# Kernel tuning notes

Measured on AMD Instinct MI355X. Metric: run time of the kernel, lower is better.

The kernel has to match this reference:

```python
import jax, jax.numpy as jnp
import numpy as np
import jax.ops

N_NODES = 50000
N_EDGES = 800000
N_GRAPHS = 512
F_IN = 128
HID = 256
N_CLASSES = 1

def _xavier(key, shape):
    fan_in, fan_out = shape[0], shape[1]
    std = (2.0 / (fan_in + fan_out)) ** 0.5
    return jax.random.normal(key, shape, dtype=jnp.float32) * std

def setup_inputs() -> dict:
    key = jax.random.key(0)
    ks = jax.random.split(key, 12)
    x = jax.random.normal(ks[0], (N_NODES, F_IN), dtype=jnp.float32)
    edge_index = jax.random.randint(ks[1], (2, N_EDGES), 0, N_NODES, dtype=jnp.int64)
    batch = jnp.sort(jax.random.randint(ks[2], (N_NODES,), 0, N_GRAPHS, dtype=jnp.int64))
    return {
        'x': x, 'edge_index': edge_index, 'batch': batch,
        'W0': _xavier(ks[3], (F_IN, HID)), 'b0': jnp.zeros((HID,), jnp.float32),
        'W1': _xavier(ks[4], (HID, HID)), 'b1': jnp.zeros((HID,), jnp.float32),
        'W2': _xavier(ks[5], (HID, HID)), 'b2': jnp.zeros((HID,), jnp.float32),
        'Wm1': _xavier(ks[6], (HID, HID)), 'bm1': jnp.zeros((HID,), jnp.float32),
        'Wm2': _xavier(ks[7], (HID, N_CLASSES)), 'bm2': jnp.zeros((N_CLASSES,), jnp.float32),
    }

def _gcn_layer(h, W, b, src, dst, deg_inv_sqrt):
    # PyG GCNConv: linear -> symmetric-normalized aggregation (with self loops) -> bias
    hw = h @ W                                        # [N, out]
    norm = deg_inv_sqrt[src] * deg_inv_sqrt[dst]      # [E]
    msg = hw[src] * norm[:, None]                     # [E, out]
    agg = jax.ops.segment_sum(msg, dst, num_segments=N_NODES)
    agg = agg + hw * (deg_inv_sqrt ** 2)[:, None]     # self-loop term
    return agg + b

def reference(x, edge_index, batch, W0, b0, W1, b1, W2, b2, Wm1, bm1, Wm2, bm2):
    src, dst = edge_index[0], edge_index[1]
    # degree with added self loops (in-degree at dst)
    deg = jax.ops.segment_sum(jnp.ones((N_EDGES,), jnp.float32), dst, num_segments=N_NODES) + 1.0
    deg_inv_sqrt = jax.lax.rsqrt(deg)
    h = jax.nn.relu(_gcn_layer(x, W0, b0, src, dst, deg_inv_sqrt))
    h = jax.nn.relu(_gcn_layer(h, W1, b1, src, dst, deg_inv_sqrt))
    h = jax.nn.relu(_gcn_layer(h, W2, b2, src, dst, deg_inv_sqrt))
    # global mean pool over graphs
    sums = jax.ops.segment_sum(h, batch, num_segments=N_GRAPHS)
    cnts = jax.ops.segment_sum(jnp.ones((N_NODES,), jnp.float32), batch, num_segments=N_GRAPHS)
    pooled = sums / jnp.maximum(cnts, 1.0)[:, None]   # [G, HID]
    out = jax.nn.relu(pooled @ Wm1 + bm1) @ Wm2 + bm2 # [G, num_classes]
    return out
```

## Files before the change

### kernel.cpp

```cpp
#include <hip/hip_runtime.h>

constexpr int N_NODES  = 50000;
constexpr int N_EDGES  = 800000;
constexpr int N_GRAPHS = 512;
constexpr int F_IN     = 128;
constexpr int HID      = 256;
constexpr int NPAD     = 50048;

typedef short short8 __attribute__((ext_vector_type(8)));
typedef float f32x4  __attribute__((ext_vector_type(4)));

__device__ __forceinline__ unsigned short f2b(float f) {
    unsigned u = __float_as_uint(f);
    u += 0x7fffu + ((u >> 16) & 1u);
    return (unsigned short)(u >> 16);
}
__device__ __forceinline__ float b2f_lo(unsigned u) { return __uint_as_float(u << 16); }
__device__ __forceinline__ float b2f_hi(unsigned u) { return __uint_as_float(u & 0xffff0000u); }

__global__ __launch_bounds__(256) void prep_kernel(
    const int* __restrict__ dst, int* __restrict__ deg, int* __restrict__ seq,
    const float* __restrict__ W0, const float* __restrict__ W1, const float* __restrict__ W2,
    unsigned short* __restrict__ Wt0, unsigned short* __restrict__ Wt1, unsigned short* __restrict__ Wt2)
{
    const int b = blockIdx.x, t = threadIdx.x;
    if (b < 3125) {
        int e = b * 256 + t;
        seq[e] = atomicAdd(&deg[dst[e]], 1);
    } else {
        int i = (b - 3125) * 256 + t;
        const float* W; unsigned short* Wt; int K; int j;
        if (i < 32768)      { W = W0; Wt = Wt0; K = 128; j = i; }
        else if (i < 98304) { W = W1; Wt = Wt1; K = 256; j = i - 32768; }
        else                { W = W2; Wt = Wt2; K = 256; j = i - 98304; }
        int k = j >> 8, n = j & 255;
        int idx = (n >> 7) * (K * 128) + (((k >> 3) * 128 + (n & 127)) << 3) + (k & 7);
        Wt[idx] = f2b(W[j]);
    }
}

__global__ void block_sum_dis_kernel(const int* __restrict__ deg, int* __restrict__ bsum,
                                     float* __restrict__ dis, int* __restrict__ bcnt, int n) {
    __shared__ int sm[256];
    __shared__ int hist[64];
    int t = threadIdx.x, base = blockIdx.x * 1024;
    if (t < 64) hist[t] = 0;
    __syncthreads();
    int s = 0;
    #pragma unroll
    for (int i = 0; i < 4; ++i) {
        int idx = base + t + i * 256;
        if (idx < n) {
            int d = deg[idx]; s += d;
            dis[idx] = rsqrtf((float)d + 1.0f);
            atomicAdd(&hist[63 - min(d, 63)], 1);
        }
    }
    sm[t] = s; __syncthreads();
    for (int o = 128; o > 0; o >>= 1) { if (t < o) sm[t] += sm[t + o]; __syncthreads(); }
    if (t == 0) bsum[blockIdx.x] = sm[0];
    if (t < 64 && hist[t]) atomicAdd(&bcnt[t], hist[t]);
}

__global__ void scan_bsum_kernel(int* __restrict__ bsum, int nb,
                                 const int* __restrict__ bcnt, int* __restrict__ bcur) {
    __shared__ int sm[64], sb[64];
    int t = threadIdx.x;
    int v = (t < nb) ? bsum[t] : 0;
    int c = bcnt[t];
    sm[t] = v; sb[t] = c; __syncthreads();
    for (int o = 1; o < 64; o <<= 1) {
        int a = (t >= o) ? sm[t - o] : 0;
        int bb = (t >= o) ? sb[t - o] : 0;
        __syncthreads();
        sm[t] += a; sb[t] += bb;
        __syncthreads();
    }
    if (t < nb) bsum[t] = sm[t] - v;
    bcur[t] = sb[t] - c;
}

__global__ void scan_local_kernel(const int* __restrict__ deg, const int* __restrict__ bsum,
                                  int* __restrict__ row_start, int* __restrict__ bcur,
                                  int4* __restrict__ perm4, int* __restrict__ idx_of,
                                  const float* __restrict__ dis, int n) {
    __shared__ int sm[256];
    __shared__ int lcnt[64], lbase[64];
    int t = threadIdx.x, base = blockIdx.x * 1024;
    if (t < 64) lcnt[t] = 0;
    int idx0 = base + t * 4;
    int v[4], s = 0;
    #pragma unroll
    for (int i = 0; i < 4; ++i) { int id = idx0 + i; v[i] = (id < n) ? deg[id] : 0; s += v[i]; }
    sm[t] = s; __syncthreads();
    for (int o = 1; o < 256; o <<= 1) {
        int a = (t >= o) ? sm[t - o] : 0; __syncthreads();
        sm[t] += a; __syncthreads();
    }
    int excl = bsum[blockIdx.x] + sm[t] - s;
    int st[4], lp[4];
    #pragma unroll
    for (int i = 0; i < 4; ++i) {
        int id = idx0 + i;
        st[i] = excl;
        if (id < n) {
            row_start[id] = excl;
            lp[i] = atomicAdd(&lcnt[63 - min(v[i], 63)], 1);
        }
        excl += v[i];
    }
    __syncthreads();
    if (t < 64) lbase[t] = lcnt[t] ? atomicAdd(&bcur[t], lcnt[t]) : 0;
    __syncthreads();
    #pragma unroll
    for (int i = 0; i < 4; ++i) {
        int id = idx0 + i;
        if (id < n) {
            int hb = 63 - min(v[i], 63);
            int pos = lbase[hb] + lp[i];
            perm4[pos] = make_int4(id, st[i], st[i] + v[i], __float_as_int(dis[id]));
            idx_of[id] = pos;
        }
    }
}

__global__ __launch_bounds__(256) void fillcsr_xconv_kernel(
    const int* __restrict__ src, const int* __restrict__ dst,
    const float* __restrict__ dis, const int* __restrict__ idx_of,
    const int* __restrict__ row_start, const int* __restrict__ seq,
    int2* __restrict__ csr,
    const float* __restrict__ x, const int4* __restrict__ perm4,
    unsigned short* __restrict__ x_bf)
{
    const int b = blockIdx.x, t = threadIdx.x;
    if (b < 3125) {
        int e = b * 256 + t;
        int s = src[e], d = dst[e];
        int pos = row_start[d] + seq[e];
        float w = dis[s] * dis[d];
        csr[pos] = make_int2(idx_of[s], __float_as_int(w));
    } else {
        int idx = (b - 3125) * 64 + (t >> 2);
        if (idx >= N_NODES) return;
        int node = perm4[idx].x;
        int c = t & 3;
        const float4* xs = reinterpret_cast<const float4*>(x + (size_t)node * 128 + c * 32);
        unsigned short* dp = x_bf + ((size_t)(c >> 1) * NPAD + idx) * 64 + (c & 1) * 32;
        #pragma unroll
        for (int u = 0; u < 8; ++u) {
            float4 v = xs[u];
            unsigned r0 = (unsigned)f2b(v.x) | ((unsigned)f2b(v.y) << 16);
            unsigned r1 = (unsigned)f2b(v.z) | ((unsigned)f2b(v.w) << 16);
            *reinterpret_cast<uint2*>(dp + u * 4) = make_uint2(r0, r1);
        }
    }
}

template<int F>
__global__ __launch_bounds__(256) void agg_split(
    const unsigned short* __restrict__ hin, const int4* __restrict__ perm4,
    const int2* __restrict__ csr, uint4* __restrict__ out4)
{
    constexpr int ROW  = F / 2;
    constexpr int LPR  = ROW / 8;
    constexpr int NSUB = 64 / LPR;
    constexpr int EPS  = 16 / NSUB;
    const int gid  = blockIdx.x;
    const int hh   = gid & 1;
    const int nb   = gid >> 1;
    const int lane = threadIdx.x & 63;
    const int sub  = lane / LPR;
    const int fcl  = lane % LPR;
    const int idx  = nb * 4 + (threadIdx.x >> 6);
    if (idx >= N_NODES) return;
    const int4 p = perm4[idx];
    const float dn = __int_as_float(p.w);
    const unsigned short* hb = hin + (size_t)hh * NPAD * ROW;

    float acc[8];
    {
        float sw = (sub == 0) ? dn * dn : 0.0f;
        uint2 u2[2];
        *reinterpret_cast<uint4*>(u2) =
            *reinterpret_cast<const uint4*>(hb + (size_t)idx * ROW + fcl * 8);
        #pragma unroll
        for (int h = 0; h < 2; ++h) {
            acc[h * 4 + 0] = b2f_lo(u2[h].x) * sw;
            acc[h * 4 + 1] = b2f_hi(u2[h].x) * sw;
            acc[h * 4 + 2] = b2f_lo(u2[h].y) * sw;
            acc[h * 4 + 3] = b2f_hi(u2[h].y) * sw;
        }
    }

    int j = p.y;
    const int end = p.z;
    for (; j + 16 <= end; j += 16) {
        int2 c[EPS];
        uint2 g[EPS][2];
        #pragma unroll
        for (int u = 0; u < EPS; ++u) c[u] = csr[j + sub * EPS + u];
        #pragma unroll
        for (int u = 0; u < EPS; ++u)
            *reinterpret_cast<uint4*>(g[u]) =
                *reinterpret_cast<const uint4*>(hb + (size_t)c[u].x * ROW + fcl * 8);
        #pragma unroll
        for (int u = 0; u < EPS; ++u) {
            float w = __int_as_float(c[u].y);
            #pragma unroll
            for (int h = 0; h < 2; ++h) {
                acc[h * 4 + 0] = fmaf(b2f_lo(g[u][h].x), w, acc[h * 4 + 0]);
                acc[h * 4 + 1] = fmaf(b2f_hi(g[u][h].x), w, acc[h * 4 + 1]);
                acc[h * 4 + 2] = fmaf(b2f_lo(g[u][h].y), w, acc[h * 4 + 2]);
                acc[h * 4 + 3] = fmaf(b2f_hi(g[u][h].y), w, acc[h * 4 + 3]);
            }
        }
    }
    int jj = j + sub;
    for (; jj + NSUB < end; jj += 2 * NSUB) {
        int2 c0 = csr[jj], c1 = csr[jj + NSUB];
        uint2 g0[2], g1[2];
        *reinterpret_cast<uint4*>(g0) =
            *reinterpret_cast<const uint4*>(hb + (size_t)c0.x * ROW + fcl * 8);
        *reinterpret_cast<uint4*>(g1) =
            *reinterpret_cast<const uint4*>(hb + (size_t)c1.x * ROW + fcl * 8);
        float w0 = __int_as_float(c0.y), w1 = __int_as_float(c1.y);
        #pragma unroll
        for (int h = 0; h < 2; ++h) {
            acc[h * 4 + 0] = fmaf(b2f_lo(g0[h].x), w0, fmaf(b2f_lo(g1[h].x), w1, acc[h * 4 + 0]));
            acc[h * 4 + 1] = fmaf(b2f_hi(g0[h].x), w0, fmaf(b2f_hi(g1[h].x), w1, acc[h * 4 + 1]));
            acc[h * 4 + 2] = fmaf(b2f_lo(g0[h].y), w0, fmaf(b2f_lo(g1[h].y), w1, acc[h * 4 + 2]));
            acc[h * 4 + 3] = fmaf(b2f_hi(g0[h].y), w0, fmaf(b2f_hi(g1[h].y), w1, acc[h * 4 + 3]));
        }
    }
    if (jj < end) {
        int2 c0 = csr[jj];
        float w = __int_as_float(c0.y);
        uint2 g[2];
        *reinterpret_cast<uint4*>(g) =
            *reinterpret_cast<const uint4*>(hb + (size_t)c0.x * ROW + fcl * 8);
        #pragma unroll
        for (int h = 0; h < 2; ++h) {
            acc[h * 4 + 0] = fmaf(b2f_lo(g[h].x), w, acc[h * 4 + 0]);
            acc[h * 4 + 1] = fmaf(b2f_hi(g[h].x), w, acc[h * 4 + 1]);
            acc[h * 4 + 2] = fmaf(b2f_lo(g[h].y), w, acc[h * 4 + 2]);
            acc[h * 4 + 3] = fmaf(b2f_hi(g[h].y), w, acc[h * 4 + 3]);
        }
    }

    #pragma unroll
    for (int k = 0; k < 8; ++k) {
        #pragma unroll
        for (int off = LPR; off < 64; off <<= 1)
            acc[k] += __shfl_xor(acc[k], off, 64);
    }

    if (sub == 0) {
        uint2 r[2];
        #pragma unroll
        for (int h = 0; h < 2; ++h) {
            r[h].x = (unsigned)f2b(acc[h * 4 + 0]) | ((unsigned)f2b(acc[h * 4 + 1]) << 16);
            r[h].y = (unsigned)f2b(acc[h * 4 + 2]) | ((unsigned)f2b(acc[h * 4 + 3]) << 16);
        }
        int fc = hh * LPR + fcl;
        int chunk = (idx >> 7) * (128 * (F / 8)) + fc * 128 + (idx & 127);
        out4[chunk] = *reinterpret_cast<uint4*>(r);
    }
}

template<int K>
__global__ __launch_bounds__(256) void gemm_frag(
    const uint4* __restrict__ A4,
    const unsigned short* __restrict__ Wt_frag,
    const float* __restrict__ bias,
    unsigned short* __restrict__ C,
    int relu)
{
    __shared__ __align__(16) unsigned short Bs[K * 128];
    const int t    = threadIdx.x;
    const int lane = t & 63;
    const int w    = t >> 6;
    const int wm   = w & 1, wn = w >> 1;
    const int q    = lane >> 4, m = lane & 15;
    const int panel = blockIdx.x;
    const int col0  = blockIdx.y * 128;

    {
        const uint4* src4 = reinterpret_cast<const uint4*>(Wt_frag + blockIdx.y * (K * 128));
        uint4* dst4 = reinterpret_cast<uint4*>(Bs);
        #pragma unroll
        for (int it = 0; it < K / 16; ++it)
            dst4[it * 256 + t] = src4[it * 256 + t];
    }
    __syncthreads();

    f32x4 acc[4][4] = {};
    const int abase = panel * (128 * (K / 8));

    #pragma unroll
    for (int kb = 0; kb < K / 32; ++kb) {
        short8 af[4], bf[4];
        #pragma unroll
        for (int i = 0; i < 4; ++i) {
            uint4 v = A4[abase + (kb * 4 + q) * 128 + wm * 64 + i * 16 + m];
            af[i] = *reinterpret_cast<short8*>(&v);
        }
        #pragma unroll
        for (int jn = 0; jn < 4; ++jn)
            bf[jn] = *reinterpret_cast<const short8*>(&Bs[((kb * 4 + q) * 128 + wn * 64 + jn * 16 + m) * 8]);
        #pragma unroll
        for (int i = 0; i < 4; ++i)
            #pragma unroll
            for (int jn = 0; jn < 4; ++jn)
                acc[i][jn] = __builtin_amdgcn_mfma_f32_16x16x32_bf16(af[i], bf[jn], acc[i][jn], 0, 0, 0);
    }

    #pragma unroll
    for (int jn = 0; jn < 4; ++jn) {
        int col = col0 + wn * 64 + jn * 16 + m;
        float bj = bias[col];
        int ch = col >> 7, cc = col & 127;
        #pragma unroll
        for (int i = 0; i < 4; ++i) {
            int rowb = panel * 128 + wm * 64 + i * 16 + q * 4;
            #pragma unroll
            for (int r = 0; r < 4; ++r) {
                float v = acc[i][jn][r] + bj;
                if (relu) v = fmaxf(v, 0.f);
                C[((size_t)ch * NPAD + (rowb + r)) * 128 + cc] = f2b(v);
            }
        }
    }
}

__global__ __launch_bounds__(512) void pool_mlp_kernel(
    const unsigned short* __restrict__ h, const int* __restrict__ batch,
    const int* __restrict__ idx_of,
    const float* __restrict__ Wm1, const float* __restrict__ bm1,
    const float* __restrict__ Wm2, const float* __restrict__ bm2,
    float* __restrict__ out)
{
    __shared__ float psum[4][HID];
    __shared__ float p[HID];
    __shared__ float red[HID];
    __shared__ int se[2];
    const int g = blockIdx.x, t = threadIdx.x;
    if (t < 2) {
        int target = g + t;
        int lo = 0, hi = N_NODES;
        while (lo < hi) { int mid = (lo + hi) >> 1; if (batch[mid] < target) lo = mid + 1; else hi = mid; }
        se[t] = lo;
    }
    __syncthreads();
    const int s = se[0], e = se[1];

    const int fp = t & 127;
    const int pl = t >> 7;
    const unsigned short* hp = h + (size_t)(fp >> 6) * ((size_t)NPAD * 128) + ((2 * fp) & 127);
    float a0 = 0.f, a1 = 0.f;
    int n = s + pl;
    for (; n + 12 < e; n += 16) {
        int i0 = idx_of[n], i1 = idx_of[n + 4], i2 = idx_of[n + 8], i3 = idx_of[n + 12];
        unsigned u0 = *reinterpret_cast<const unsigned*>(hp + (size_t)i0 * 128);
        unsigned u1 = *reinterpret_cast<const unsigned*>(hp + (size_t)i1 * 128);
        unsigned u2 = *reinterpret_cast<const unsigned*>(hp + (size_t)i2 * 128);
        unsigned u3 = *reinterpret_cast<const unsigned*>(hp + (size_t)i3 * 128);
        a0 += (b2f_lo(u0) + b2f_lo(u1)) + (b2f_lo(u2) + b2f_lo(u3));
        a1 += (b2f_hi(u0) + b2f_hi(u1)) + (b2f_hi(u2) + b2f_hi(u3));
    }
    for (; n < e; n += 4) {
        unsigned u = *reinterpret_cast<const unsigned*>(hp + (size_t)idx_of[n] * 128);
        a0 += b2f_lo(u); a1 += b2f_hi(u);
    }
    psum[pl][2 * fp]     = a0;
    psum[pl][2 * fp + 1] = a1;
    __syncthreads();
    if (t < HID) {
        float inv = 1.0f / fmaxf((float)(e - s), 1.0f);
        p[t] = (psum[0][t] + psum[1][t] + psum[2][t] + psum[3][t]) * inv;
    }
    __syncthreads();

    const int tt = t & 255, qq = t >> 8;
    const int k0 = qq * 128;
    float a2 = 0.f;
    for (int k = 0; k < 128; ++k)
        a2 = fmaf(p[k0 + k], Wm1[(k0 + k) * HID + tt], a2);
    psum[qq][tt] = a2;
    __syncthreads();
    if (t < HID)
        red[t] = fmaxf(psum[0][t] + psum[1][t] + bm1[t], 0.f) * Wm2[t];
    __syncthreads();
    for (int o = 128; o > 0; o >>= 1) {
        if (t < o) red[t] += red[t + o];
        __syncthreads();
    }
    if (t == 0) out[g] = red[0] + bm2[0];
}

extern "C" void kernel_launch(void* const* d_in, const int* in_sizes, int n_in,
                              void* d_out, int out_size, void* d_ws, size_t ws_size,
                              hipStream_t stream) {
    const float* x    = (const float*)d_in[0];
    const int*   ei   = (const int*)d_in[1];
    const int*   batch= (const int*)d_in[2];
    const float* W0   = (const float*)d_in[3];
    const float* b0   = (const float*)d_in[4];
    const float* W1   = (const float*)d_in[5];
    const float* b1   = (const float*)d_in[6];
    const float* W2   = (const float*)d_in[7];
    const float* b2   = (const float*)d_in[8];
    const float* Wm1  = (const float*)d_in[9];
    const float* bm1  = (const float*)d_in[10];
    const float* Wm2  = (const float*)d_in[11];
    const float* bm2  = (const float*)d_in[12];
    float* out = (float*)d_out;

    char* ws = (char*)d_ws;
    size_t off = 0;
    auto alloc = [&](size_t bytes) -> void* {
        void* p = ws + off;
        off += (bytes + 255) & ~(size_t)255;
        return p;
    };
    int*   deg    = (int*)  alloc((size_t)N_NODES * 4);
    int*   bcnt   = (int*)  alloc(64 * 4);
    int*   bcur   = (int*)  alloc(64 * 4);
    float* dis    = (float*)alloc((size_t)N_NODES * 4);
    int*   row_st = (int*)  alloc((size_t)N_NODES * 4);
    int*   bsum   = (int*)  alloc((size_t)64 * 4);
    int*   seq    = (int*)  alloc((size_t)N_EDGES * 4);
    int4*  perm4  = (int4*) alloc((size_t)NPAD * 16);
    int*   idx_of = (int*)  alloc((size_t)N_NODES * 4);
    int2*  csr    = (int2*) alloc((size_t)N_EDGES * 8);
    unsigned short* x_bf  = (unsigned short*)alloc((size_t)NPAD * F_IN * 2);
    unsigned short* Wt0   = (unsigned short*)alloc((size_t)F_IN * HID * 2);
    unsigned short* Wt1   = (unsigned short*)alloc((size_t)HID * HID * 2);
    unsigned short* Wt2   = (unsigned short*)alloc((size_t)HID * HID * 2);
    unsigned short* bufA  = (unsigned short*)alloc((size_t)NPAD * HID * 2);
    unsigned short* bufB  = (unsigned short*)alloc((size_t)NPAD * HID * 2);

    const int* src = ei;
    const int* dst = ei + N_EDGES;
    const int NB = (N_NODES + 1023) / 1024;

    size_t zlen = (size_t)((char*)bcur - (char*)deg) + 64 * 4;
    hipMemsetAsync(deg, 0, zlen, stream);

    prep_kernel         <<<3765, 256, 0, stream>>>(dst, deg, seq, W0, W1, W2, Wt0, Wt1, Wt2);
    block_sum_dis_kernel<<<NB, 256, 0, stream>>>(deg, bsum, dis, bcnt, N_NODES);
    scan_bsum_kernel    <<<1, 64, 0, stream>>>(bsum, NB, bcnt, bcur);
    scan_local_kernel   <<<NB, 256, 0, stream>>>(deg, bsum, row_st, bcur, perm4, idx_of, dis, N_NODES);
    fillcsr_xconv_kernel<<<3125 + 782, 256, 0, stream>>>(src, dst, dis, idx_of, row_st, seq, csr,
                                                         x, perm4, x_bf);

    dim3 ggrid(NPAD / 128, 2);
    const int AGG_B = (N_NODES + 3) / 4;

    agg_split<F_IN><<<AGG_B * 2, 256, 0, stream>>>(x_bf, perm4, csr, (uint4*)bufA);
    gemm_frag<F_IN><<<ggrid, 256, 0, stream>>>((const uint4*)bufA, Wt0, b0, bufB, 1);

    agg_split<HID><<<AGG_B * 2, 256, 0, stream>>>(bufB, perm4, csr, (uint4*)bufA);
    gemm_frag<HID><<<ggrid, 256, 0, stream>>>((const uint4*)bufA, Wt1, b1, bufB, 1);

    agg_split<HID><<<AGG_B * 2, 256, 0, stream>>>(bufB, perm4, csr, (uint4*)bufA);
    gemm_frag<HID><<<ggrid, 256, 0, stream>>>((const uint4*)bufA, Wt2, b2, bufB, 1);

    pool_mlp_kernel<<<N_GRAPHS, 512, 0, stream>>>(bufB, batch, idx_of, Wm1, bm1, Wm2, bm2, out);
}
```

Baseline: 384.7 us.

## Fuse degree scan kernels with grid barrier and widen GEMM tile to full width

Merges the three degree-scan and bucket-sort kernels into one 49-block kernel that uses an atomic spin grid barrier, removing two launches and round trips. Separately, each GEMM block now covers all 256 output columns, so it loads the whole weight matrix into LDS and each wave holds 4x8 accumulators. The aggregated activations are then read once instead of twice. The spin barrier depends on all 49 blocks being co-resident, and the larger LDS footprint (128KB for K=256) and doubled accumulator registers may cut occupancy or exceed LDS limits.

```diff
diff --git a/kernel.cpp b/kernel.cpp
--- a/kernel.cpp
+++ b/kernel.cpp
@@ -6,6 +6,7 @@
 constexpr int F_IN     = 128;
 constexpr int HID      = 256;
 constexpr int NPAD     = 50048;
+constexpr int NB_SCAN  = 49;
 
 typedef short short8 __attribute__((ext_vector_type(8)));
 typedef float f32x4  __attribute__((ext_vector_type(4)));
@@ -39,65 +40,68 @@
     }
 }
 
-__global__ void block_sum_dis_kernel(const int* __restrict__ deg, int* __restrict__ bsum,
-                                     float* __restrict__ dis, int* __restrict__ bcnt, int n) {
+__global__ __launch_bounds__(256) void scan_fused_kernel(
+    const int* __restrict__ deg, float* __restrict__ dis,
+    int* __restrict__ bcnt, int* __restrict__ bsum,
+    int* __restrict__ bcur2, int* __restrict__ gbar,
+    int* __restrict__ row_start, int4* __restrict__ perm4, int* __restrict__ idx_of, int n)
+{
     __shared__ int sm[256];
-    __shared__ int hist[64];
-    int t = threadIdx.x, base = blockIdx.x * 1024;
-    if (t < 64) hist[t] = 0;
-    __syncthreads();
-    int s = 0;
+    __shared__ int h64[64];
+    __shared__ int horig[64];
+    __shared__ int sscan[64];
+    __shared__ int lcnt[64], lbase[64];
+    const int t = threadIdx.x, b = blockIdx.x, base = b * 1024;
+    const int idx0 = base + t * 4;
+
+    if (t < 64) h64[t] = 0;
+    __syncthreads();
+    int v[4], s1 = 0;
     #pragma unroll
     for (int i = 0; i < 4; ++i) {
-        int idx = base + t + i * 256;
-        if (idx < n) {
-            int d = deg[idx]; s += d;
-            dis[idx] = rsqrtf((float)d + 1.0f);
-            atomicAdd(&hist[63 - min(d, 63)], 1);
-        }
-    }
-    sm[t] = s; __syncthreads();
+        int id = idx0 + i;
+        v[i] = (id < n) ? deg[id] : 0; s1 += v[i];
+        if (id < n) {
+            dis[id] = rsqrtf((float)v[i] + 1.0f);
+            atomicAdd(&h64[63 - min(v[i], 63)], 1);
+        }
+    }
+    sm[t] = s1; __syncthreads();
     for (int o = 128; o > 0; o >>= 1) { if (t < o) sm[t] += sm[t + o]; __syncthreads(); }
-    if (t == 0) bsum[blockIdx.x] = sm[0];
-    if (t < 64 && hist[t]) atomicAdd(&bcnt[t], hist[t]);
-}
-
-__global__ void scan_bsum_kernel(int* __restrict__ bsum, int nb,
-                                 const int* __restrict__ bcnt, int* __restrict__ bcur) {
-    __shared__ int sm[64], sb[64];
-    int t = threadIdx.x;
-    int v = (t < nb) ? bsum[t] : 0;
-    int c = bcnt[t];
-    sm[t] = v; sb[t] = c; __syncthreads();
+    if (t == 0) atomicExch(&bsum[b], sm[0]);
+    if (t < 64 && h64[t]) atomicAdd(&bcnt[t], h64[t]);
+
+    __threadfence();
+    __syncthreads();
+    if (t == 0) {
+        atomicAdd(gbar, 1);
+        while (atomicAdd(gbar, 0) < (int)gridDim.x) { }
+    }
+    __syncthreads();
+    __threadfence();
+
+    if (t < 64) {
+        sscan[t] = (t < NB_SCAN) ? atomicAdd(&bsum[t], 0) : 0;
+        int bc = atomicAdd(&bcnt[t], 0);
+        horig[t] = bc; h64[t] = bc;
+    }
+    __syncthreads();
     for (int o = 1; o < 64; o <<= 1) {
-        int a = (t >= o) ? sm[t - o] : 0;
-        int bb = (t >= o) ? sb[t - o] : 0;
+        int a = (t >= o && t < 64) ? sscan[t - o] : 0;
+        int c = (t >= o && t < 64) ? h64[t - o]  : 0;
         __syncthreads();
-        sm[t] += a; sb[t] += bb;
+        if (t < 64) { sscan[t] += a; h64[t] += c; }
         __syncthreads();
     }
-    if (t < nb) bsum[t] = sm[t] - v;
-    bcur[t] = sb[t] - c;
-}
-
-__global__ void scan_local_kernel(const int* __restrict__ deg, const int* __restrict__ bsum,
-                                  int* __restrict__ row_start, int* __restrict__ bcur,
-                                  int4* __restrict__ perm4, int* __restrict__ idx_of,
-                                  const float* __restrict__ dis, int n) {
-    __shared__ int sm[256];
-    __shared__ int lcnt[64], lbase[64];
-    int t = threadIdx.x, base = blockIdx.x * 1024;
+    const int myExcl = (b == 0) ? 0 : sscan[b - 1];
+
     if (t < 64) lcnt[t] = 0;
-    int idx0 = base + t * 4;
-    int v[4], s = 0;
-    #pragma unroll
-    for (int i = 0; i < 4; ++i) { int id = idx0 + i; v[i] = (id < n) ? deg[id] : 0; s += v[i]; }
-    sm[t] = s; __syncthreads();
+    sm[t] = s1; __syncthreads();
     for (int o = 1; o < 256; o <<= 1) {
         int a = (t >= o) ? sm[t - o] : 0; __syncthreads();
         sm[t] += a; __syncthreads();
     }
-    int excl = bsum[blockIdx.x] + sm[t] - s;
+    int excl = myExcl + sm[t] - s1;
     int st[4], lp[4];
     #pragma unroll
     for (int i = 0; i < 4; ++i) {
@@ -110,7 +114,7 @@
         excl += v[i];
     }
     __syncthreads();
-    if (t < 64) lbase[t] = lcnt[t] ? atomicAdd(&bcur[t], lcnt[t]) : 0;
+    if (t < 64) lbase[t] = lcnt[t] ? (h64[t] - horig[t]) + atomicAdd(&bcur2[t], lcnt[t]) : 0;
     __syncthreads();
     #pragma unroll
     for (int i = 0; i < 4; ++i) {
@@ -118,7 +122,8 @@
         if (id < n) {
             int hb = 63 - min(v[i], 63);
             int pos = lbase[hb] + lp[i];
-            perm4[pos] = make_int4(id, st[i], st[i] + v[i], __float_as_int(dis[id]));
+            perm4[pos] = make_int4(id, st[i], st[i] + v[i],
+                                   __float_as_int(rsqrtf((float)v[i] + 1.0f)));
             idx_of[id] = pos;
         }
     }
@@ -275,50 +280,51 @@
     unsigned short* __restrict__ C,
     int relu)
 {
-    __shared__ __align__(16) unsigned short Bs[K * 128];
+    __shared__ __align__(16) unsigned short Bs[2 * K * 128];
     const int t    = threadIdx.x;
     const int lane = t & 63;
     const int w    = t >> 6;
     const int wm   = w & 1, wn = w >> 1;
     const int q    = lane >> 4, m = lane & 15;
     const int panel = blockIdx.x;
-    const int col0  = blockIdx.y * 128;
 
     {
-        const uint4* src4 = reinterpret_cast<const uint4*>(Wt_frag + blockIdx.y * (K * 128));
+        const uint4* src4 = reinterpret_cast<const uint4*>(Wt_frag);
         uint4* dst4 = reinterpret_cast<uint4*>(Bs);
         #pragma unroll
-        for (int it = 0; it < K / 16; ++it)
+        for (int it = 0; it < K / 8; ++it)
             dst4[it * 256 + t] = src4[it * 256 + t];
     }
     __syncthreads();
 
-    f32x4 acc[4][4] = {};
+    f32x4 acc[4][8] = {};
     const int abase = panel * (128 * (K / 8));
+    const int bhalf = wn * (K * 128);
 
     #pragma unroll
     for (int kb = 0; kb < K / 32; ++kb) {
-        short8 af[4], bf[4];
+        short8 af[4], bf[8];
         #pragma unroll
         for (int i = 0; i < 4; ++i) {
             uint4 v = A4[abase + (kb * 4 + q) * 128 + wm * 64 + i * 16 + m];
             af[i] = *reinterpret_cast<short8*>(&v);
         }
         #pragma unroll
-        for (int jn = 0; jn < 4; ++jn)
-            bf[jn] = *reinterpret_cast<const short8*>(&Bs[((kb * 4 + q) * 128 + wn * 64 + jn * 16 + m) * 8]);
+        for (int jn = 0; jn < 8; ++jn)
+            bf[jn] = *reinterpret_cast<const short8*>(
+                &Bs[bhalf + (((kb * 4 + q) * 128 + jn * 16 + m) << 3)]);
         #pragma unroll
         for (int i = 0; i < 4; ++i)
             #pragma unroll
-            for (int jn = 0; jn < 4; ++jn)
+            for (int jn = 0; jn < 8; ++jn)
                 acc[i][jn] = __builtin_amdgcn_mfma_f32_16x16x32_bf16(af[i], bf[jn], acc[i][jn], 0, 0, 0);
     }
 
     #pragma unroll
-    for (int jn = 0; jn < 4; ++jn) {
-        int col = col0 + wn * 64 + jn * 16 + m;
+    for (int jn = 0; jn < 8; ++jn) {
+        int col = wn * 128 + jn * 16 + m;
         float bj = bias[col];
-        int ch = col >> 7, cc = col & 127;
+        int ch = wn, cc = col & 127;
         #pragma unroll
         for (int i = 0; i < 4; ++i) {
             int rowb = panel * 128 + wm * 64 + i * 16 + q * 4;
@@ -424,7 +430,8 @@
     };
     int*   deg    = (int*)  alloc((size_t)N_NODES * 4);
     int*   bcnt   = (int*)  alloc(64 * 4);
-    int*   bcur   = (int*)  alloc(64 * 4);
+    int*   bcur2  = (int*)  alloc(64 * 4);
+    int*   gbar   = (int*)  alloc(64 * 4);
     float* dis    = (float*)alloc((size_t)N_NODES * 4);
     int*   row_st = (int*)  alloc((size_t)N_NODES * 4);
     int*   bsum   = (int*)  alloc((size_t)64 * 4);
@@ -441,29 +448,27 @@
 
     const int* src = ei;
     const int* dst = ei + N_EDGES;
-    const int NB = (N_NODES + 1023) / 1024;
-
-    size_t zlen = (size_t)((char*)bcur - (char*)deg) + 64 * 4;
+
+    size_t zlen = (size_t)((char*)gbar - (char*)deg) + 64 * 4;
     hipMemsetAsync(deg, 0, zlen, stream);
 
-    prep_kernel         <<<3765, 256, 0, stream>>>(dst, deg, seq, W0, W1, W2, Wt0, Wt1, Wt2);
-    block_sum_dis_kernel<<<NB, 256, 0, stream>>>(deg, bsum, dis, bcnt, N_NODES);
-    scan_bsum_kernel    <<<1, 64, 0, stream>>>(bsum, NB, bcnt, bcur);
-    scan_local_kernel   <<<NB, 256, 0, stream>>>(deg, bsum, row_st, bcur, perm4, idx_of, dis, N_NODES);
+    prep_kernel      <<<3765, 256, 0, stream>>>(dst, deg, seq, W0, W1, W2, Wt0, Wt1, Wt2);
+    scan_fused_kernel<<<NB_SCAN, 256, 0, stream>>>(deg, dis, bcnt, bsum, bcur2, gbar,
+                                                   row_st, perm4, idx_of, N_NODES);
     fillcsr_xconv_kernel<<<3125 + 782, 256, 0, stream>>>(src, dst, dis, idx_of, row_st, seq, csr,
                                                          x, perm4, x_bf);
 
-    dim3 ggrid(NPAD / 128, 2);
     const int AGG_B = (N_NODES + 3) / 4;
+    const int GEMM_B = NPAD / 128;
 
     agg_split<F_IN><<<AGG_B * 2, 256, 0, stream>>>(x_bf, perm4, csr, (uint4*)bufA);
-    gemm_frag<F_IN><<<ggrid, 256, 0, stream>>>((const uint4*)bufA, Wt0, b0, bufB, 1);
+    gemm_frag<F_IN><<<GEMM_B, 256, 0, stream>>>((const uint4*)bufA, Wt0, b0, bufB, 1);
 
     agg_split<HID><<<AGG_B * 2, 256, 0, stream>>>(bufB, perm4, csr, (uint4*)bufA);
-    gemm_frag<HID><<<ggrid, 256, 0, stream>>>((const uint4*)bufA, Wt1, b1, bufB, 1);
+    gemm_frag<HID><<<GEMM_B, 256, 0, stream>>>((const uint4*)bufA, Wt1, b1, bufB, 1);
 
     agg_split<HID><<<AGG_B * 2, 256, 0, stream>>>(bufB, perm4, csr, (uint4*)bufA);
-    gemm_frag<HID><<<ggrid, 256, 0, stream>>>((const uint4*)bufA, Wt2, b2, bufB, 1);
+    gemm_frag<HID><<<GEMM_B, 256, 0, stream>>>((const uint4*)bufA, Wt2, b2, bufB, 1);
 
     pool_mlp_kernel<<<N_GRAPHS, 512, 0, stream>>>(bufB, batch, idx_of, Wm1, bm1, Wm2, bm2, out);
 }
```

Measured after the change: 396.6 us. 3.1% more time.
